# Kernel tuning notes

Hardware: AMD Instinct MI355X
Metric: run time of the kernel (lower is better)

The kernel has to match this reference:

```python
import jax, jax.numpy as jnp
import numpy as np

D, N_T, N, N_H = 8, 2048, 64, 8
STD_E = 0.02
STD_Q = 0.02


def setup_inputs() -> dict:
    key = jax.random.key(0)
    k1, k2, k3 = jax.random.split(key, 3)
    r_prime = jax.random.normal(k1, (D, N_T, N), dtype=jnp.float32)
    Q = jax.random.normal(k2, (N_H, N, N), dtype=jnp.float32) * STD_Q
    E = jax.random.normal(k3, (N_H, N, N), dtype=jnp.float32) * STD_E
    return {"r_prime": r_prime, "Q": Q, "E": E}


def reference(r_prime, Q, E):
    # r_prime: (b=d, t=n_t, i=n); Q, E: (h, i, j)
    n_t = r_prime.shape[1]
    # Omega[b,h,t,u] = sum_ij r'[b,t,i] Q[h,i,j] r'[b,u,j]
    Qr = jnp.einsum('hij,buj->bhui', Q, r_prime)          # (b, h, u, i)
    Omega = jnp.einsum('bti,bhui->bhtu', r_prime, Qr)     # (b, h, t, u)
    # causal lower-triangular mask (t >= u)
    mask = jnp.tril(jnp.ones((n_t, n_t), dtype=r_prime.dtype))
    Omega = Omega * mask  # broadcast over (b, h)
    # r[b,t,i] = sum_{h,u,j} Omega[b,h,t,u] E[h,i,j] r'[b,u,j]
    Er = jnp.einsum('hij,buj->bhui', E, r_prime)          # (b, h, u, i)
    r = jnp.einsum('bhtu,bhui->bti', Omega, Er)           # (b, t, i)
    return r
```

## Files before the change

kernel.cpp:

```cpp
#include <hip/hip_runtime.h>

#define D_B 8
#define N_T 2048
#define NN  64
#define N_H 8
#define N_C 32
#define NP  72

typedef __bf16 bf16;
typedef bf16 bf16x8 __attribute__((ext_vector_type(8)));
typedef bf16 bf16x4 __attribute__((ext_vector_type(4)));
typedef float f32x4 __attribute__((ext_vector_type(4)));

static __device__ __forceinline__ f32x4 mfma16(bf16x8 a, bf16x8 b, f32x4 c) {
    return __builtin_amdgcn_mfma_f32_16x16x32_bf16(a, b, c, 0, 0, 0);
}

static __device__ __forceinline__ bf16x8 ldcvt8(const float* p) {
    const f32x4 v0 = *(const f32x4*)p;
    const f32x4 v1 = *(const f32x4*)(p + 4);
    bf16x8 r;
#pragma unroll
    for (int k = 0; k < 4; k++) { r[k] = (bf16)v0[k]; r[4 + k] = (bf16)v1[k]; }
    return r;
}

__global__ __launch_bounds__(256, 4) void k_dg(
    const float* __restrict__ rp, const float* __restrict__ Qm,
    const float* __restrict__ Em,
    bf16* __restrict__ dGq, bf16* __restrict__ Rbf,
    bf16* __restrict__ Qrd, bf16* __restrict__ Erd)
{
    __shared__ bf16 Ql[64 * NP];
    __shared__ bf16 El[64 * NP];
    __shared__ bf16 QT[64 * NP];
    __shared__ bf16 ET[64 * NP];
    const int b = blockIdx.x, c = blockIdx.y, qt = blockIdx.z;
    const int tid = threadIdx.x;
    const int w = tid >> 6, l = tid & 63, q = l >> 4, l16 = l & 15;
    const int row = tid >> 2, col = (tid & 3) * 16;

    const float* rrow = rp + ((size_t)b * N_T + c * 64 + w * 16 + l16) * NN;
    const bf16x8 a0 = ldcvt8(rrow + q * 8);
    const bf16x8 a1 = ldcvt8(rrow + 32 + q * 8);

    if (qt == 0) {
        const float* src = rp + ((size_t)b * N_T + c * 64 + row) * NN + col;
        bf16* d = Rbf + ((size_t)b * N_T + c * 64 + row) * NN + col;
        *(bf16x8*)d       = ldcvt8(src);
        *(bf16x8*)(d + 8) = ldcvt8(src + 8);
    }

    f32x4 dacc[4];
#pragma unroll
    for (int ns = 0; ns < 4; ns++) { f32x4 z = {0.f, 0.f, 0.f, 0.f}; dacc[ns] = z; }

    for (int hh = 0; hh < 2; hh++) {
        const int h = qt * 2 + hh;
        {
            const float* qs = Qm + (size_t)h * 4096 + row * 64 + col;
            const float* es = Em + (size_t)h * 4096 + row * 64 + col;
            *(bf16x8*)&Ql[row * NP + col]     = ldcvt8(qs);
            *(bf16x8*)&Ql[row * NP + col + 8] = ldcvt8(qs + 8);
            *(bf16x8*)&El[row * NP + col]     = ldcvt8(es);
            *(bf16x8*)&El[row * NP + col + 8] = ldcvt8(es + 8);
        }
        __syncthreads();
        const size_t tb = (((size_t)(b * N_C + c)) * N_H + h) * 4096;
#pragma unroll
        for (int ns = 0; ns < 4; ns++) {
            bf16x8 b0 = *(const bf16x8*)&Ql[(ns * 16 + l16) * NP + q * 8];
            bf16x8 b1 = *(const bf16x8*)&Ql[(ns * 16 + l16) * NP + 32 + q * 8];
            f32x4 z = {0.f, 0.f, 0.f, 0.f};
            f32x4 s = mfma16(a0, b0, z);
            s = mfma16(a1, b1, s);
            bf16x4 p;
#pragma unroll
            for (int r = 0; r < 4; r++) p[r] = (bf16)s[r];
#pragma unroll
            for (int r = 0; r < 4; r++)
                Qrd[tb + (w * 16 + q * 4 + r) * 64 + ns * 16 + l16] = p[r];
            *(bf16x4*)&QT[(ns * 16 + l16) * NP + w * 16 + q * 4] = p;
            b0 = *(const bf16x8*)&El[(ns * 16 + l16) * NP + q * 8];
            b1 = *(const bf16x8*)&El[(ns * 16 + l16) * NP + 32 + q * 8];
            f32x4 s2 = mfma16(a0, b0, z);
            s2 = mfma16(a1, b1, s2);
#pragma unroll
            for (int r = 0; r < 4; r++) p[r] = (bf16)s2[r];
            *(bf16x4*)&ET[(ns * 16 + l16) * NP + w * 16 + q * 4] = p;
        }
        __syncthreads();
        {
            const bf16x8 qa0 = *(const bf16x8*)&QT[(w * 16 + l16) * NP + q * 8];
            const bf16x8 qa1 = *(const bf16x8*)&QT[(w * 16 + l16) * NP + 32 + q * 8];
#pragma unroll
            for (int ns = 0; ns < 4; ns++) {
                const bf16x8 e0 = *(const bf16x8*)&ET[(ns * 16 + l16) * NP + q * 8];
                const bf16x8 e1 = *(const bf16x8*)&ET[(ns * 16 + l16) * NP + 32 + q * 8];
                dacc[ns] = mfma16(qa0, e0, dacc[ns]);
                dacc[ns] = mfma16(qa1, e1, dacc[ns]);
            }
        }
        {
            const bf16x8 v0 = *(const bf16x8*)&ET[row * NP + col];
            const bf16x8 v1 = *(const bf16x8*)&ET[row * NP + col + 8];
            bf16* d = Erd + tb + row * 64 + col;
            *(bf16x8*)d = v0;
            *(bf16x8*)(d + 8) = v1;
        }
        __syncthreads();
    }
#pragma unroll
    for (int ns = 0; ns < 4; ns++) {
        bf16x4 p;
#pragma unroll
        for (int r = 0; r < 4; r++) p[r] = (bf16)dacc[ns][r];
        *(bf16x4*)&QT[(ns * 16 + l16) * NP + w * 16 + q * 4] = p;
    }
    __syncthreads();
    {
        bf16* dst = dGq + (((size_t)(b * N_C + c)) * 4 + qt) * 4096 + row * 64 + col;
        *(bf16x8*)dst       = *(const bf16x8*)&QT[row * NP + col];
        *(bf16x8*)(dst + 8) = *(const bf16x8*)&QT[row * NP + col + 8];
    }
}

__global__ __launch_bounds__(256, 4) void k_fold(const bf16* __restrict__ dGq,
                                                 bf16* __restrict__ dG8)
{
    const int b = blockIdx.x, c = blockIdx.y;
    const size_t base = ((size_t)(b * N_C + c)) * 4 * 4096 + threadIdx.x * 16;
    float s[16];
#pragma unroll
    for (int k = 0; k < 16; k++) s[k] = 0.f;
#pragma unroll
    for (int qt = 0; qt < 4; qt++) {
        const bf16x8 v0 = *(const bf16x8*)(dGq + base + (size_t)qt * 4096);
        const bf16x8 v1 = *(const bf16x8*)(dGq + base + (size_t)qt * 4096 + 8);
#pragma unroll
        for (int k = 0; k < 8; k++) { s[k] += (float)v0[k]; s[8 + k] += (float)v1[k]; }
    }
    bf16x8 o0, o1;
#pragma unroll
    for (int k = 0; k < 8; k++) { o0[k] = (bf16)s[k]; o1[k] = (bf16)s[8 + k]; }
    bf16* dst = dG8 + (size_t)(b * N_C + c) * 4096 + threadIdx.x * 16;
    *(bf16x8*)dst = o0;
    *(bf16x8*)(dst + 8) = o1;
}

__global__ __launch_bounds__(256, 4) void k_scan(const bf16* __restrict__ dG8,
                                                 bf16* __restrict__ Gc)
{
    const int b = blockIdx.x, c = blockIdx.y;
    const int tid = threadIdx.x;
    float run[16];
#pragma unroll
    for (int k = 0; k < 16; k++) run[k] = 0.f;
    const bf16* base = dG8 + (size_t)b * N_C * 4096 + tid * 16;
    int t = 0;
    for (; t + 4 <= c; t += 4) {
        bf16x8 v[4][2];
#pragma unroll
        for (int j = 0; j < 4; j++) {
            v[j][0] = *(const bf16x8*)(base + (size_t)(t + j) * 4096);
            v[j][1] = *(const bf16x8*)(base + (size_t)(t + j) * 4096 + 8);
        }
#pragma unroll
        for (int j = 0; j < 4; j++)
#pragma unroll
            for (int k = 0; k < 8; k++) {
                run[k] += (float)v[j][0][k];
                run[8 + k] += (float)v[j][1][k];
            }
    }
    for (; t < c; t++) {
        const bf16x8 v0 = *(const bf16x8*)(base + (size_t)t * 4096);
        const bf16x8 v1 = *(const bf16x8*)(base + (size_t)t * 4096 + 8);
#pragma unroll
        for (int k = 0; k < 8; k++) { run[k] += (float)v0[k]; run[8 + k] += (float)v1[k]; }
    }
    bf16x8 o0, o1;
#pragma unroll
    for (int k = 0; k < 8; k++) { o0[k] = (bf16)run[k]; o1[k] = (bf16)run[8 + k]; }
    bf16* dst = Gc + (size_t)(b * N_C + c) * 4096 + tid * 16;
    *(bf16x8*)dst = o0;
    *(bf16x8*)(dst + 8) = o1;
}

template <int NU>
static __device__ __forceinline__ void head_iter(
    const bf16* __restrict__ Qh, const bf16* __restrict__ Eh,
    bf16* __restrict__ Sw, const bf16x8 ra0, const bf16x8 ra1,
    int l16, int q, int tbase, f32x4 (&acc)[4])
{
#pragma unroll
    for (int nu = 0; nu < NU; nu++) {
        const bf16x8 b0 = *(const bf16x8*)&Qh[(nu * 16 + l16) * 64 + q * 8];
        const bf16x8 b1 = *(const bf16x8*)&Qh[(nu * 16 + l16) * 64 + 32 + q * 8];
        f32x4 z = {0.f, 0.f, 0.f, 0.f};
        f32x4 sv = mfma16(ra0, b0, z);
        sv = mfma16(ra1, b1, sv);
        const int u_loc = nu * 16 + l16;
#pragma unroll
        for (int r = 0; r < 4; r++) {
            const int t_loc = tbase + q * 4 + r;
            Sw[(q * 4 + r) * NP + u_loc] = (u_loc <= t_loc) ? (bf16)sv[r] : (bf16)0.f;
        }
    }
    const bf16x8 sa0 = *(const bf16x8*)&Sw[l16 * NP + q * 8];
#pragma unroll
    for (int ns = 0; ns < 4; ns++) {
        const bf16x8 e0 = *(const bf16x8*)&Eh[(ns * 16 + l16) * 64 + q * 8];
        acc[ns] = mfma16(sa0, e0, acc[ns]);
    }
    if (NU == 4) {
        const bf16x8 sa1 = *(const bf16x8*)&Sw[l16 * NP + 32 + q * 8];
#pragma unroll
        for (int ns = 0; ns < 4; ns++) {
            const bf16x8 e1 = *(const bf16x8*)&Eh[(ns * 16 + l16) * 64 + 32 + q * 8];
            acc[ns] = mfma16(sa1, e1, acc[ns]);
        }
    }
}

__global__ __launch_bounds__(256, 4) void k_out(
    const bf16* __restrict__ Gc, const bf16* __restrict__ Rbf,
    const bf16* __restrict__ Qrd, const bf16* __restrict__ Erd,
    float* __restrict__ out)
{
    __shared__ bf16 Sl[4 * 2 * 16 * NP];
    __shared__ float Ob[32 * 65];
    const int b = blockIdx.x, c = blockIdx.y, half = blockIdx.z;
    const int tid = threadIdx.x;
    const int w = tid >> 6, l = tid & 63, q = l >> 4, l16 = l & 15;
    const int s = w & 1, g = w >> 1;

    const int trow = c * 64 + half * 32 + s * 16 + l16;
    const bf16x8 ra0 = *(const bf16x8*)&Rbf[((size_t)b * N_T + trow) * NN + q * 8];
    const bf16x8 ra1 = *(const bf16x8*)&Rbf[((size_t)b * N_T + trow) * NN + 32 + q * 8];

    bf16* Sw0 = Sl + (w * 2 + 0) * 16 * NP;
    bf16* Sw1 = Sl + (w * 2 + 1) * 16 * NP;
    const int tbase = half * 32 + s * 16;
    const size_t hb = (((size_t)(b * N_C + c)) * N_H + g * 4) * 4096;
    const bf16* Qg = Qrd + hb;
    const bf16* Eg = Erd + hb;
    f32x4 acc[4];
#pragma unroll
    for (int ns = 0; ns < 4; ns++) { f32x4 z = {0.f, 0.f, 0.f, 0.f}; acc[ns] = z; }

    if (half) {
#pragma unroll
        for (int hh = 0; hh < 4; hh++)
            head_iter<4>(Qg + (size_t)hh * 4096, Eg + (size_t)hh * 4096,
                         (hh & 1) ? Sw1 : Sw0, ra0, ra1, l16, q, tbase, acc);
    } else {
#pragma unroll
        for (int hh = 0; hh < 4; hh++)
            head_iter<2>(Qg + (size_t)hh * 4096, Eg + (size_t)hh * 4096,
                         (hh & 1) ? Sw1 : Sw0, ra0, ra1, l16, q, tbase, acc);
    }

    if (g == 1) {
        const bf16* Gt = Gc + (size_t)(b * N_C + c) * 4096;
#pragma unroll
        for (int ns = 0; ns < 4; ns++) {
            const bf16x8 g0 = *(const bf16x8*)&Gt[(ns * 16 + l16) * 64 + q * 8];
            const bf16x8 g1 = *(const bf16x8*)&Gt[(ns * 16 + l16) * 64 + 32 + q * 8];
            acc[ns] = mfma16(ra0, g0, acc[ns]);
            acc[ns] = mfma16(ra1, g1, acc[ns]);
        }
    }
    if (g == 0) {
#pragma unroll
        for (int ns = 0; ns < 4; ns++)
#pragma unroll
            for (int r = 0; r < 4; r++)
                Ob[(s * 16 + q * 4 + r) * 65 + ns * 16 + l16] = acc[ns][r];
    }
    __syncthreads();
    if (g == 1) {
        const int t0 = c * 64 + half * 32;
#pragma unroll
        for (int ns = 0; ns < 4; ns++)
#pragma unroll
            for (int r = 0; r < 4; r++) {
                const float sum = acc[ns][r] + Ob[(s * 16 + q * 4 + r) * 65 + ns * 16 + l16];
                out[((size_t)b * N_T + t0 + s * 16 + q * 4 + r) * NN + ns * 16 + l16] = sum;
            }
    }
}

extern "C" void kernel_launch(void* const* d_in, const int* in_sizes, int n_in,
                              void* d_out, int out_size, void* d_ws, size_t ws_size,
                              hipStream_t stream) {
    const float* rp = (const float*)d_in[0];
    const float* Qm = (const float*)d_in[1];
    const float* Em = (const float*)d_in[2];
    float* out = (float*)d_out;

    bf16* dGq = (bf16*)d_ws;
    bf16* dG8 = dGq + (size_t)D_B * N_C * 4 * 4096;
    bf16* Gc  = dG8 + (size_t)D_B * N_C * 4096;
    bf16* Rbf = Gc + (size_t)D_B * N_C * 4096;
    bf16* Qrd = Rbf + (size_t)D_B * N_T * NN;
    bf16* Erd = Qrd + (size_t)D_B * N_C * N_H * 4096;

    k_dg<<<dim3(D_B, N_C, 4), 256, 0, stream>>>(rp, Qm, Em, dGq, Rbf, Qrd, Erd);
    k_fold<<<dim3(D_B, N_C), 256, 0, stream>>>(dGq, dG8);
    k_scan<<<dim3(D_B, N_C), 256, 0, stream>>>(dG8, Gc);
    k_out<<<dim3(D_B, N_C, 2), 256, 0, stream>>>(Gc, Rbf, Qrd, Erd, out);
}
```

Baseline: 104.8 us.

## Fuse fold into prefix scan and split output kernel over column halves

Removes the separate fold kernel: the scan now reads the per-quarter partial G deltas directly and sums 4*c slices, unrolled by 8. The output kernel grid doubles, with each block computing only half of the 64 output columns. This cuts one launch and its intermediate buffer, and doubles block count for occupancy. In exchange the scan reads four times as many slices, and the Q-side score computation is duplicated across the two column-half blocks.

```diff
diff --git a/kernel.cpp b/kernel.cpp
--- a/kernel.cpp
+++ b/kernel.cpp
@@ -125,55 +125,33 @@
     }
 }
 
-__global__ __launch_bounds__(256, 4) void k_fold(const bf16* __restrict__ dGq,
-                                                 bf16* __restrict__ dG8)
-{
-    const int b = blockIdx.x, c = blockIdx.y;
-    const size_t base = ((size_t)(b * N_C + c)) * 4 * 4096 + threadIdx.x * 16;
-    float s[16];
-#pragma unroll
-    for (int k = 0; k < 16; k++) s[k] = 0.f;
-#pragma unroll
-    for (int qt = 0; qt < 4; qt++) {
-        const bf16x8 v0 = *(const bf16x8*)(dGq + base + (size_t)qt * 4096);
-        const bf16x8 v1 = *(const bf16x8*)(dGq + base + (size_t)qt * 4096 + 8);
-#pragma unroll
-        for (int k = 0; k < 8; k++) { s[k] += (float)v0[k]; s[8 + k] += (float)v1[k]; }
-    }
-    bf16x8 o0, o1;
-#pragma unroll
-    for (int k = 0; k < 8; k++) { o0[k] = (bf16)s[k]; o1[k] = (bf16)s[8 + k]; }
-    bf16* dst = dG8 + (size_t)(b * N_C + c) * 4096 + threadIdx.x * 16;
-    *(bf16x8*)dst = o0;
-    *(bf16x8*)(dst + 8) = o1;
-}
-
-__global__ __launch_bounds__(256, 4) void k_scan(const bf16* __restrict__ dG8,
-                                                 bf16* __restrict__ Gc)
+__global__ __launch_bounds__(256, 4) void k_scanq(const bf16* __restrict__ dGq,
+                                                  bf16* __restrict__ Gc)
 {
     const int b = blockIdx.x, c = blockIdx.y;
     const int tid = threadIdx.x;
     float run[16];
 #pragma unroll
     for (int k = 0; k < 16; k++) run[k] = 0.f;
-    const bf16* base = dG8 + (size_t)b * N_C * 4096 + tid * 16;
+    const bf16* base = dGq + (size_t)b * N_C * 4 * 4096 + tid * 16;
+    const int nt = 4 * c;
     int t = 0;
-    for (; t + 4 <= c; t += 4) {
-        bf16x8 v[4][2];
-#pragma unroll
-        for (int j = 0; j < 4; j++) {
+    for (; t + 8 <= nt; t += 8) {
+        bf16x8 v[8][2];
+#pragma unroll
+        for (int j = 0; j < 8; j++) {
             v[j][0] = *(const bf16x8*)(base + (size_t)(t + j) * 4096);
             v[j][1] = *(const bf16x8*)(base + (size_t)(t + j) * 4096 + 8);
         }
 #pragma unroll
-        for (int j = 0; j < 4; j++)
+        for (int j = 0; j < 8; j++)
 #pragma unroll
             for (int k = 0; k < 8; k++) {
                 run[k] += (float)v[j][0][k];
                 run[8 + k] += (float)v[j][1][k];
             }
     }
-    for (; t < c; t++) {
+    for (; t < nt; t++) {
         const bf16x8 v0 = *(const bf16x8*)(base + (size_t)t * 4096);
         const bf16x8 v1 = *(const bf16x8*)(base + (size_t)t * 4096 + 8);
 #pragma unroll
@@ -191,7 +169,7 @@
 static __device__ __forceinline__ void head_iter(
     const bf16* __restrict__ Qh, const bf16* __restrict__ Eh,
     bf16* __restrict__ Sw, const bf16x8 ra0, const bf16x8 ra1,
-    int l16, int q, int tbase, f32x4 (&acc)[4])
+    int l16, int q, int tbase, int io, f32x4 (&acc)[2])
 {
 #pragma unroll
     for (int nu = 0; nu < NU; nu++) {
@@ -209,15 +187,15 @@
     }
     const bf16x8 sa0 = *(const bf16x8*)&Sw[l16 * NP + q * 8];
 #pragma unroll
-    for (int ns = 0; ns < 4; ns++) {
-        const bf16x8 e0 = *(const bf16x8*)&Eh[(ns * 16 + l16) * 64 + q * 8];
+    for (int ns = 0; ns < 2; ns++) {
+        const bf16x8 e0 = *(const bf16x8*)&Eh[(io + ns * 16 + l16) * 64 + q * 8];
         acc[ns] = mfma16(sa0, e0, acc[ns]);
     }
     if (NU == 4) {
         const bf16x8 sa1 = *(const bf16x8*)&Sw[l16 * NP + 32 + q * 8];
 #pragma unroll
-        for (int ns = 0; ns < 4; ns++) {
-            const bf16x8 e1 = *(const bf16x8*)&Eh[(ns * 16 + l16) * 64 + 32 + q * 8];
+        for (int ns = 0; ns < 2; ns++) {
+            const bf16x8 e1 = *(const bf16x8*)&Eh[(io + ns * 16 + l16) * 64 + 32 + q * 8];
             acc[ns] = mfma16(sa1, e1, acc[ns]);
         }
     }
@@ -229,8 +207,9 @@
     float* __restrict__ out)
 {
     __shared__ bf16 Sl[4 * 2 * 16 * NP];
-    __shared__ float Ob[32 * 65];
-    const int b = blockIdx.x, c = blockIdx.y, half = blockIdx.z;
+    __shared__ float Ob[32 * 33];
+    const int b = blockIdx.x, c = blockIdx.y, z = blockIdx.z;
+    const int half = z >> 1, nh = z & 1;
     const int tid = threadIdx.x;
     const int w = tid >> 6, l = tid & 63, q = l >> 4, l16 = l & 15;
     const int s = w & 1, g = w >> 1;
@@ -242,51 +221,52 @@
     bf16* Sw0 = Sl + (w * 2 + 0) * 16 * NP;
     bf16* Sw1 = Sl + (w * 2 + 1) * 16 * NP;
     const int tbase = half * 32 + s * 16;
+    const int io = nh * 32;
     const size_t hb = (((size_t)(b * N_C + c)) * N_H + g * 4) * 4096;
     const bf16* Qg = Qrd + hb;
     const bf16* Eg = Erd + hb;
-    f32x4 acc[4];
-#pragma unroll
-    for (int ns = 0; ns < 4; ns++) { f32x4 z = {0.f, 0.f, 0.f, 0.f}; acc[ns] = z; }
+    f32x4 acc[2];
+#pragma unroll
+    for (int ns = 0; ns < 2; ns++) { f32x4 zz = {0.f, 0.f, 0.f, 0.f}; acc[ns] = zz; }
 
     if (half) {
 #pragma unroll
         for (int hh = 0; hh < 4; hh++)
             head_iter<4>(Qg + (size_t)hh * 4096, Eg + (size_t)hh * 4096,
-                         (hh & 1) ? Sw1 : Sw0, ra0, ra1, l16, q, tbase, acc);
+                         (hh & 1) ? Sw1 : Sw0, ra0, ra1, l16, q, tbase, io, acc);
     } else {
 #pragma unroll
         for (int hh = 0; hh < 4; hh++)
             head_iter<2>(Qg + (size_t)hh * 4096, Eg + (size_t)hh * 4096,
-                         (hh & 1) ? Sw1 : Sw0, ra0, ra1, l16, q, tbase, acc);
+                         (hh & 1) ? Sw1 : Sw0, ra0, ra1, l16, q, tbase, io, acc);
     }
 
     if (g == 1) {
         const bf16* Gt = Gc + (size_t)(b * N_C + c) * 4096;
 #pragma unroll
-        for (int ns = 0; ns < 4; ns++) {
-            const bf16x8 g0 = *(const bf16x8*)&Gt[(ns * 16 + l16) * 64 + q * 8];
-            const bf16x8 g1 = *(const bf16x8*)&Gt[(ns * 16 + l16) * 64 + 32 + q * 8];
+        for (int ns = 0; ns < 2; ns++) {
+            const bf16x8 g0 = *(const bf16x8*)&Gt[(io + ns * 16 + l16) * 64 + q * 8];
+            const bf16x8 g1 = *(const bf16x8*)&Gt[(io + ns * 16 + l16) * 64 + 32 + q * 8];
             acc[ns] = mfma16(ra0, g0, acc[ns]);
             acc[ns] = mfma16(ra1, g1, acc[ns]);
         }
     }
     if (g == 0) {
 #pragma unroll
-        for (int ns = 0; ns < 4; ns++)
+        for (int ns = 0; ns < 2; ns++)
 #pragma unroll
             for (int r = 0; r < 4; r++)
-                Ob[(s * 16 + q * 4 + r) * 65 + ns * 16 + l16] = acc[ns][r];
+                Ob[(s * 16 + q * 4 + r) * 33 + ns * 16 + l16] = acc[ns][r];
     }
     __syncthreads();
     if (g == 1) {
         const int t0 = c * 64 + half * 32;
 #pragma unroll
-        for (int ns = 0; ns < 4; ns++)
+        for (int ns = 0; ns < 2; ns++)
 #pragma unroll
             for (int r = 0; r < 4; r++) {
-                const float sum = acc[ns][r] + Ob[(s * 16 + q * 4 + r) * 65 + ns * 16 + l16];
-                out[((size_t)b * N_T + t0 + s * 16 + q * 4 + r) * NN + ns * 16 + l16] = sum;
+                const float sum = acc[ns][r] + Ob[(s * 16 + q * 4 + r) * 33 + ns * 16 + l16];
+                out[((size_t)b * N_T + t0 + s * 16 + q * 4 + r) * NN + io + ns * 16 + l16] = sum;
             }
     }
 }
@@ -300,14 +280,12 @@
     float* out = (float*)d_out;
 
     bf16* dGq = (bf16*)d_ws;
-    bf16* dG8 = dGq + (size_t)D_B * N_C * 4 * 4096;
-    bf16* Gc  = dG8 + (size_t)D_B * N_C * 4096;
+    bf16* Gc  = dGq + (size_t)D_B * N_C * 4 * 4096;
     bf16* Rbf = Gc + (size_t)D_B * N_C * 4096;
     bf16* Qrd = Rbf + (size_t)D_B * N_T * NN;
     bf16* Erd = Qrd + (size_t)D_B * N_C * N_H * 4096;
 
     k_dg<<<dim3(D_B, N_C, 4), 256, 0, stream>>>(rp, Qm, Em, dGq, Rbf, Qrd, Erd);
-    k_fold<<<dim3(D_B, N_C), 256, 0, stream>>>(dGq, dG8);
-    k_scan<<<dim3(D_B, N_C), 256, 0, stream>>>(dG8, Gc);
-    k_out<<<dim3(D_B, N_C, 2), 256, 0, stream>>>(Gc, Rbf, Qrd, Erd, out);
-}
+    k_scanq<<<dim3(D_B, N_C), 256, 0, stream>>>(dGq, Gc);
+    k_out<<<dim3(D_B, N_C, 4), 256, 0, stream>>>(Gc, Rbf, Qrd, Erd, out);
+}
```

Measured after the change: 136.6 us. 1.3x slower.
